# Performance work log

Measured on AMD Instinct MI355X. Metric: run time of the kernel, lower is better.

The kernel has to match this reference:

```python
import jax, jax.numpy as jnp
import numpy as np

N = 50000   # total nodes
E = 600000  # total edges
D = 128     # feature dim (node_dim == all gcn_dims)
G = 128     # graphs in batch
LN_EPS = 1e-5


def setup_inputs() -> dict:
    key = jax.random.key(0)
    ks = jax.random.split(key, 16)
    inp = {
        "x": jax.random.normal(ks[0], (N, D), dtype=jnp.float32),
        "edge_index": jax.random.randint(ks[1], (2, E), 0, N),
        "batch": jnp.sort(jax.random.randint(ks[2], (N,), 0, G)),
    }
    for l in range(3):
        inp[f"W{l}"] = jax.random.normal(ks[3 + 4 * l], (D, D), dtype=jnp.float32) / np.float32(np.sqrt(D))
        inp[f"b{l}"] = jnp.zeros((D,), jnp.float32)
        inp[f"g{l}"] = jnp.ones((D,), jnp.float32)   # LayerNorm weight
        inp[f"be{l}"] = jnp.zeros((D,), jnp.float32)  # LayerNorm bias
    return inp


def _gcn_norm(edge_index):
    # PyG GCNConv default: add self-loops, symmetric deg^-1/2 normalization.
    loop = jnp.arange(N, dtype=edge_index.dtype)
    src = jnp.concatenate([edge_index[0], loop])
    dst = jnp.concatenate([edge_index[1], loop])
    deg = jax.ops.segment_sum(jnp.ones(src.shape[0], jnp.float32), dst, num_segments=N)
    dinv = jnp.where(deg > 0, jax.lax.rsqrt(deg), 0.0)
    norm = dinv[src] * dinv[dst]  # [E+N]
    return src, dst, norm


def _block(x, src, dst, norm, W, b, g, be):
    # GCNConv: gather-transform-scatter
    h = x @ W                                   # [N, D]
    msg = h[src] * norm[:, None]                # [E+N, D] gather + scale
    out = jax.ops.segment_sum(msg, dst, num_segments=N) + b
    # LayerNorm
    mu = jnp.mean(out, axis=-1, keepdims=True)
    var = jnp.mean((out - mu) ** 2, axis=-1, keepdims=True)
    out = (out - mu) * jax.lax.rsqrt(var + LN_EPS) * g + be
    # residual (Identity since in==out channels) + SiLU
    return jax.nn.silu(out + x)


def reference(x, edge_index, batch, W0, b0, g0, be0, W1, b1, g1, be1, W2, b2, g2, be2):
    src, dst, norm = _gcn_norm(edge_index)
    params = [(W0, b0, g0, be0), (W1, b1, g1, be1), (W2, b2, g2, be2)]
    for (W, b, g, be) in params:
        x = _block(x, src, dst, norm, W, b, g, be)
    # global mean pool over batch ids
    counts = jax.ops.segment_sum(jnp.ones((N,), jnp.float32), batch, num_segments=G)
    sums = jax.ops.segment_sum(x, batch, num_segments=G)
    return sums / jnp.maximum(counts, 1.0)[:, None]
```

## Files before the change

kernel.cpp:

```cpp
#include <hip/hip_runtime.h>
#include <math.h>

#define DD 128

typedef __attribute__((ext_vector_type(8))) short short8;
typedef __attribute__((ext_vector_type(4))) float f32x4;

__device__ __forceinline__ unsigned short f2b(float f) {
    unsigned int x = __float_as_uint(f);
    return (unsigned short)((x + 0x7FFFu + ((x >> 16) & 1u)) >> 16);
}
__device__ __forceinline__ float b2f(unsigned short u) {
    return __uint_as_float(((unsigned int)u) << 16);
}

__global__ __launch_bounds__(256) void k_count(const int* __restrict__ dst, int* __restrict__ cnt, int E) {
    int e = blockIdx.x * 256 + threadIdx.x;
    if (e < E) atomicAdd(&cnt[dst[e]], 1);
}

__global__ __launch_bounds__(256) void k_scan1(const int* __restrict__ cnt, int* __restrict__ part, int N) {
    __shared__ int lds[256];
    int t = threadIdx.x;
    int i = blockIdx.x * 256 + t;
    lds[t] = (i < N) ? cnt[i] : 0;
    __syncthreads();
#pragma unroll
    for (int off = 128; off > 0; off >>= 1) {
        if (t < off) lds[t] += lds[t + off];
        __syncthreads();
    }
    if (t == 0) part[blockIdx.x] = lds[0];
}

__global__ __launch_bounds__(1024) void k_scan2(int* __restrict__ part, int* __restrict__ rowptr,
                                                int nblk, int N) {
    __shared__ int lds[1024];
    int t = threadIdx.x;
    int v = (t < nblk) ? part[t] : 0;
    lds[t] = v;
    __syncthreads();
    for (int off = 1; off < 1024; off <<= 1) {
        int u = (t >= off) ? lds[t - off] : 0;
        __syncthreads();
        lds[t] += u;
        __syncthreads();
    }
    if (t < nblk) part[t] = lds[t] - v;
    if (t == 1023) rowptr[N] = lds[1023];
}

__global__ __launch_bounds__(256) void k_scan3(const int* __restrict__ cnt, const int* __restrict__ part,
                                               int* __restrict__ rowptr, int N) {
    __shared__ int lds[256];
    int t = threadIdx.x;
    int i = blockIdx.x * 256 + t;
    int v = (i < N) ? cnt[i] : 0;
    lds[t] = v;
    __syncthreads();
    for (int off = 1; off < 256; off <<= 1) {
        int u = (t >= off) ? lds[t - off] : 0;
        __syncthreads();
        lds[t] += u;
        __syncthreads();
    }
    if (i < N) rowptr[i] = part[blockIdx.x] + lds[t] - v;
}

__global__ __launch_bounds__(256) void k_dinv(const int* __restrict__ cnt, float* __restrict__ dinv, int N) {
    int i = blockIdx.x * 256 + threadIdx.x;
    if (i < N) dinv[i] = rsqrtf((float)cnt[i] + 1.0f);
}

__global__ __launch_bounds__(256) void k_fill(const int* __restrict__ src, const int* __restrict__ dst,
                                              const float* __restrict__ dinv, const int* __restrict__ rowptr,
                                              int* __restrict__ cursor, int2* __restrict__ adj, int E) {
    int e = blockIdx.x * 256 + threadIdx.x;
    if (e >= E) return;
    int s = src[e], d = dst[e];
    int pos = atomicAdd(&cursor[d], 1);
    float w = dinv[s] * dinv[d];
    adj[rowptr[d] + pos] = make_int2(s, __float_as_int(w));
}

__global__ __launch_bounds__(256) void k_prepW(const float* __restrict__ W, unsigned short* __restrict__ WT) {
    int idx = blockIdx.x * 256 + threadIdx.x;
    int k = idx >> 7, c = idx & 127;
    WT[c * DD + k] = f2b(W[idx]);
}

__global__ __launch_bounds__(256) void k_gemm_mfma(const float* __restrict__ X,
                                                   const unsigned short* __restrict__ WT,
                                                   unsigned short* __restrict__ H, int N) {
    __shared__ __align__(16) unsigned short sB[DD * DD];
    __shared__ __align__(16) unsigned short sA[64 * DD];
    int tid = threadIdx.x;
    long row0 = (long)blockIdx.x * 64;

#pragma unroll
    for (int i = 0; i < 8; ++i) {
        int q = tid + 256 * i;
        int c = q >> 4, j = q & 15;
        short8 v = *(const short8*)(WT + q * 8);
        int byte = c * 256 + ((j * 16) ^ ((c & 7) << 4));
        *(short8*)((char*)sB + byte) = v;
    }
#pragma unroll
    for (int i = 0; i < 4; ++i) {
        int q = tid + 256 * i;
        int r = q >> 4, j = q & 15;
        float4 a0 = make_float4(0.f, 0.f, 0.f, 0.f), a1 = a0;
        if (row0 + r < N) {
            const float4* p = (const float4*)(X + (row0 + r) * DD + j * 8);
            a0 = p[0];
            a1 = p[1];
        }
        short8 v;
        v[0] = (short)f2b(a0.x); v[1] = (short)f2b(a0.y);
        v[2] = (short)f2b(a0.z); v[3] = (short)f2b(a0.w);
        v[4] = (short)f2b(a1.x); v[5] = (short)f2b(a1.y);
        v[6] = (short)f2b(a1.z); v[7] = (short)f2b(a1.w);
        int byte = r * 256 + ((j * 16) ^ ((r & 7) << 4));
        *(short8*)((char*)sA + byte) = v;
    }
    __syncthreads();

    int w = tid >> 6, l = tid & 63;
    int lr = l & 15, kg = l >> 4;
    f32x4 acc[8] = {};

#pragma unroll
    for (int step = 0; step < 4; ++step) {
        int ar = w * 16 + lr;
        int abyte = ar * 256 + ((step * 64 + kg * 16) ^ ((ar & 7) << 4));
        short8 af = *(const short8*)((const char*)sA + abyte);
#pragma unroll
        for (int ct = 0; ct < 8; ++ct) {
            int c = ct * 16 + lr;
            int bbyte = c * 256 + ((step * 64 + kg * 16) ^ ((c & 7) << 4));
            short8 bf = *(const short8*)((const char*)sB + bbyte);
            acc[ct] = __builtin_amdgcn_mfma_f32_16x16x32_bf16(af, bf, acc[ct], 0, 0, 0);
        }
    }

#pragma unroll
    for (int ct = 0; ct < 8; ++ct) {
#pragma unroll
        for (int reg = 0; reg < 4; ++reg) {
            long r = row0 + w * 16 + kg * 4 + reg;
            if (r < N) H[r * DD + ct * 16 + lr] = f2b(acc[ct][reg]);
        }
    }
}

__global__ __launch_bounds__(256) void k_agg(const unsigned short* __restrict__ h, const float* __restrict__ xin,
                                             const int* __restrict__ rowptr, const int2* __restrict__ adj,
                                             const float* __restrict__ dinv, const float* __restrict__ b,
                                             const float* __restrict__ g, const float* __restrict__ be,
                                             float* __restrict__ xout, int N) {
    int row = blockIdx.x * 4 + (threadIdx.x >> 6);
    if (row >= N) return;
    int lane = threadIdx.x & 63;
    const unsigned int* hu = (const unsigned int*)h;

    float dv = dinv[row];
    float dv2 = dv * dv;
    unsigned int us = hu[(size_t)row * 64 + lane];
    float2 bv = ((const float2*)b)[lane];
    float2 acc = make_float2(fmaf(b2f((unsigned short)(us & 0xFFFF)), dv2, bv.x),
                             fmaf(b2f((unsigned short)(us >> 16)), dv2, bv.y));

    int beg = rowptr[row], end = rowptr[row + 1];
    for (int j0 = beg; j0 < end; j0 += 64) {
        int myj = j0 + lane;
        int2 a = make_int2(0, 0);
        if (myj < end) a = adj[myj];
        int cnt = min(64, end - j0);
        int cntR = (cnt + 7) & ~7;
        for (int k0 = 0; k0 < cntR; k0 += 8) {
            unsigned int un[8];
            float wt[8];
#pragma unroll
            for (int u = 0; u < 8; ++u) {
                int s = __shfl(a.x, k0 + u, 64);
                wt[u] = __int_as_float(__shfl(a.y, k0 + u, 64));
                un[u] = hu[(size_t)s * 64 + lane];
            }
#pragma unroll
            for (int u = 0; u < 8; ++u) {
                acc.x = fmaf(wt[u], b2f((unsigned short)(un[u] & 0xFFFF)), acc.x);
                acc.y = fmaf(wt[u], b2f((unsigned short)(un[u] >> 16)), acc.y);
            }
        }
    }

    float ssum = acc.x + acc.y;
#pragma unroll
    for (int o = 32; o > 0; o >>= 1) ssum += __shfl_xor(ssum, o, 64);
    float mu = ssum * (1.0f / 128.0f);
    float dx0 = acc.x - mu, dx1 = acc.y - mu;
    float vs = dx0 * dx0 + dx1 * dx1;
#pragma unroll
    for (int o = 32; o > 0; o >>= 1) vs += __shfl_xor(vs, o, 64);
    float rstd = rsqrtf(vs * (1.0f / 128.0f) + 1e-5f);

    float2 gv = ((const float2*)g)[lane];
    float2 bev = ((const float2*)be)[lane];
    float2 xv = ((const float2*)(xin + (size_t)row * DD))[lane];
    float a0 = fmaf(dx0 * rstd, gv.x, bev.x) + xv.x;
    float a1 = fmaf(dx1 * rstd, gv.y, bev.y) + xv.y;
    a0 = a0 / (1.0f + expf(-a0));
    a1 = a1 / (1.0f + expf(-a1));
    ((float2*)(xout + (size_t)row * DD))[lane] = make_float2(a0, a1);
}

__global__ __launch_bounds__(256) void k_pool2(const float* __restrict__ x, const int* __restrict__ batch,
                                               float* __restrict__ out, int N) {
    int gi = blockIdx.x;
    int lo = 0, hi = N;
    while (lo < hi) { int m = (lo + hi) >> 1; if (batch[m] < gi) lo = m + 1; else hi = m; }
    int beg = lo;
    lo = beg; hi = N;
    while (lo < hi) { int m = (lo + hi) >> 1; if (batch[m] < gi + 1) lo = m + 1; else hi = m; }
    int end = lo;

    int tid = threadIdx.x;
    int wave = tid >> 6, lane = tid & 63;
    float2 acc = make_float2(0.f, 0.f);
    for (int r = beg + wave; r < end; r += 4) {
        float2 v = ((const float2*)(x + (size_t)r * DD))[lane];
        acc.x += v.x;
        acc.y += v.y;
    }
    __shared__ float part[4][DD];
    ((float2*)part[wave])[lane] = acc;
    __syncthreads();
    if (wave == 0) {
        float sx = 0.f, sy = 0.f;
#pragma unroll
        for (int w = 0; w < 4; ++w) {
            float2 v = ((const float2*)part[w])[lane];
            sx += v.x;
            sy += v.y;
        }
        float inv = 1.0f / fmaxf((float)(end - beg), 1.0f);
        ((float2*)(out + (size_t)gi * DD))[lane] = make_float2(sx * inv, sy * inv);
    }
}

extern "C" void kernel_launch(void* const* d_in, const int* in_sizes, int n_in,
                              void* d_out, int out_size, void* d_ws, size_t ws_size,
                              hipStream_t stream) {
    const float* x = (const float*)d_in[0];
    const int* edge = (const int*)d_in[1];
    const int* batch = (const int*)d_in[2];
    const float* W[3] = {(const float*)d_in[3], (const float*)d_in[7], (const float*)d_in[11]};
    const float* b[3] = {(const float*)d_in[4], (const float*)d_in[8], (const float*)d_in[12]};
    const float* g[3] = {(const float*)d_in[5], (const float*)d_in[9], (const float*)d_in[13]};
    const float* be[3] = {(const float*)d_in[6], (const float*)d_in[10], (const float*)d_in[14]};

    int N = in_sizes[0] / DD;
    int E = in_sizes[1] / 2;
    int G = out_size / DD;
    const int* srcI = edge;
    const int* dstI = edge + E;

    int nblk = (N + 255) / 256;

    char* ws = (char*)d_ws;
    size_t ND = (size_t)N * DD;
    float* bufX = (float*)ws;                         ws += ND * 4;
    unsigned short* bufH = (unsigned short*)ws;       ws += ND * 2;
    unsigned short* wt[3];
    for (int l = 0; l < 3; ++l) { wt[l] = (unsigned short*)ws; ws += (size_t)DD * DD * 2; }
    float* dinv = (float*)ws;                         ws += (size_t)N * 4;
    int* cnt = (int*)ws;                              ws += (size_t)N * 4;
    int* cursor = (int*)ws;                           ws += (size_t)N * 4;
    int* rowptr = (int*)ws;                           ws += (size_t)(N + 1) * 4;
    int* part = (int*)ws;                             ws += (size_t)nblk * 4;
    ws = (char*)(((uintptr_t)ws + 15) & ~(uintptr_t)15);
    int2* adj = (int2*)ws;

    hipMemsetAsync(cnt, 0, (size_t)N * 2 * 4, stream);

    k_count<<<(E + 255) / 256, 256, 0, stream>>>(dstI, cnt, E);
    k_scan1<<<nblk, 256, 0, stream>>>(cnt, part, N);
    k_scan2<<<1, 1024, 0, stream>>>(part, rowptr, nblk, N);
    k_scan3<<<nblk, 256, 0, stream>>>(cnt, part, rowptr, N);
    k_dinv<<<(N + 255) / 256, 256, 0, stream>>>(cnt, dinv, N);
    k_fill<<<(E + 255) / 256, 256, 0, stream>>>(srcI, dstI, dinv, rowptr, cursor, adj, E);
    for (int l = 0; l < 3; ++l)
        k_prepW<<<64, 256, 0, stream>>>(W[l], wt[l]);

    const float* xin = x;
    for (int l = 0; l < 3; ++l) {
        k_gemm_mfma<<<(N + 63) / 64, 256, 0, stream>>>(xin, wt[l], bufH, N);
        k_agg<<<(N + 3) / 4, 256, 0, stream>>>(bufH, xin, rowptr, adj, dinv, b[l], g[l], be[l], bufX, N);
        xin = bufX;
    }

    k_pool2<<<G, 256, 0, stream>>>(bufX, batch, (float*)d_out, N);
}
```

Baseline: 248.3 us.

## Store inter-layer activations in bf16 and merge small setup kernels

The activation buffer written by the aggregation kernel changes from fp32 to packed bf16. The next GEMM, the residual read and the final pooling now read bf16 directly, which halves activation traffic and removes the fp32-to-bf16 conversion in the GEMM load. The dinv computation is folded into the last scan kernel, and the three weight-prep launches become one, cutting launch count. The cost is lower precision in the residual path and pooled output, and layers 1 and 2 now update the activation buffer in place.

Result: faster. 240.8 us (-3.0%).

```diff
diff --git a/kernel.cpp b/kernel.cpp
--- a/kernel.cpp
+++ b/kernel.cpp
@@ -51,7 +51,7 @@
 }
 
 __global__ __launch_bounds__(256) void k_scan3(const int* __restrict__ cnt, const int* __restrict__ part,
-                                               int* __restrict__ rowptr, int N) {
+                                               int* __restrict__ rowptr, float* __restrict__ dinv, int N) {
     __shared__ int lds[256];
     int t = threadIdx.x;
     int i = blockIdx.x * 256 + t;
@@ -64,12 +64,10 @@
         lds[t] += u;
         __syncthreads();
     }
-    if (i < N) rowptr[i] = part[blockIdx.x] + lds[t] - v;
-}
-
-__global__ __launch_bounds__(256) void k_dinv(const int* __restrict__ cnt, float* __restrict__ dinv, int N) {
-    int i = blockIdx.x * 256 + threadIdx.x;
-    if (i < N) dinv[i] = rsqrtf((float)cnt[i] + 1.0f);
+    if (i < N) {
+        rowptr[i] = part[blockIdx.x] + lds[t] - v;
+        dinv[i] = rsqrtf((float)v + 1.0f);
+    }
 }
 
 __global__ __launch_bounds__(256) void k_fill(const int* __restrict__ src, const int* __restrict__ dst,
@@ -83,13 +81,19 @@
     adj[rowptr[d] + pos] = make_int2(s, __float_as_int(w));
 }
 
-__global__ __launch_bounds__(256) void k_prepW(const float* __restrict__ W, unsigned short* __restrict__ WT) {
-    int idx = blockIdx.x * 256 + threadIdx.x;
+__global__ __launch_bounds__(256) void k_prepW3(const float* __restrict__ W0, const float* __restrict__ W1,
+                                                const float* __restrict__ W2, unsigned short* __restrict__ T0,
+                                                unsigned short* __restrict__ T1, unsigned short* __restrict__ T2) {
+    int l = blockIdx.x >> 6;
+    const float* W = (l == 0) ? W0 : (l == 1) ? W1 : W2;
+    unsigned short* WT = (l == 0) ? T0 : (l == 1) ? T1 : T2;
+    int idx = (blockIdx.x & 63) * 256 + threadIdx.x;
     int k = idx >> 7, c = idx & 127;
     WT[c * DD + k] = f2b(W[idx]);
 }
 
-__global__ __launch_bounds__(256) void k_gemm_mfma(const float* __restrict__ X,
+template <int IN_BF16>
+__global__ __launch_bounds__(256) void k_gemm_mfma(const void* __restrict__ Xv,
                                                    const unsigned short* __restrict__ WT,
                                                    unsigned short* __restrict__ H, int N) {
     __shared__ __align__(16) unsigned short sB[DD * DD];
@@ -109,17 +113,23 @@
     for (int i = 0; i < 4; ++i) {
         int q = tid + 256 * i;
         int r = q >> 4, j = q & 15;
-        float4 a0 = make_float4(0.f, 0.f, 0.f, 0.f), a1 = a0;
-        if (row0 + r < N) {
-            const float4* p = (const float4*)(X + (row0 + r) * DD + j * 8);
-            a0 = p[0];
-            a1 = p[1];
-        }
         short8 v;
-        v[0] = (short)f2b(a0.x); v[1] = (short)f2b(a0.y);
-        v[2] = (short)f2b(a0.z); v[3] = (short)f2b(a0.w);
-        v[4] = (short)f2b(a1.x); v[5] = (short)f2b(a1.y);
-        v[6] = (short)f2b(a1.z); v[7] = (short)f2b(a1.w);
+        if (IN_BF16) {
+#pragma unroll
+            for (int z = 0; z < 8; ++z) v[z] = 0;
+            if (row0 + r < N) v = *(const short8*)((const unsigned short*)Xv + (row0 + r) * DD + j * 8);
+        } else {
+            float4 a0 = make_float4(0.f, 0.f, 0.f, 0.f), a1 = a0;
+            if (row0 + r < N) {
+                const float4* p = (const float4*)((const float*)Xv + (row0 + r) * DD + j * 8);
+                a0 = p[0];
+                a1 = p[1];
+            }
+            v[0] = (short)f2b(a0.x); v[1] = (short)f2b(a0.y);
+            v[2] = (short)f2b(a0.z); v[3] = (short)f2b(a0.w);
+            v[4] = (short)f2b(a1.x); v[5] = (short)f2b(a1.y);
+            v[6] = (short)f2b(a1.z); v[7] = (short)f2b(a1.w);
+        }
         int byte = r * 256 + ((j * 16) ^ ((r & 7) << 4));
         *(short8*)((char*)sA + byte) = v;
     }
@@ -153,11 +163,12 @@
     }
 }
 
-__global__ __launch_bounds__(256) void k_agg(const unsigned short* __restrict__ h, const float* __restrict__ xin,
+template <int IN_BF16>
+__global__ __launch_bounds__(256) void k_agg(const unsigned short* __restrict__ h, const void* __restrict__ xin,
                                              const int* __restrict__ rowptr, const int2* __restrict__ adj,
                                              const float* __restrict__ dinv, const float* __restrict__ b,
                                              const float* __restrict__ g, const float* __restrict__ be,
-                                             float* __restrict__ xout, int N) {
+                                             unsigned int* __restrict__ xout, int N) {
     int row = blockIdx.x * 4 + (threadIdx.x >> 6);
     if (row >= N) return;
     int lane = threadIdx.x & 63;
@@ -206,15 +217,21 @@
 
     float2 gv = ((const float2*)g)[lane];
     float2 bev = ((const float2*)be)[lane];
-    float2 xv = ((const float2*)(xin + (size_t)row * DD))[lane];
+    float2 xv;
+    if (IN_BF16) {
+        unsigned int xu = ((const unsigned int*)xin)[(size_t)row * 64 + lane];
+        xv = make_float2(b2f((unsigned short)(xu & 0xFFFF)), b2f((unsigned short)(xu >> 16)));
+    } else {
+        xv = ((const float2*)xin)[(size_t)row * 64 + lane];
+    }
     float a0 = fmaf(dx0 * rstd, gv.x, bev.x) + xv.x;
     float a1 = fmaf(dx1 * rstd, gv.y, bev.y) + xv.y;
     a0 = a0 / (1.0f + expf(-a0));
     a1 = a1 / (1.0f + expf(-a1));
-    ((float2*)(xout + (size_t)row * DD))[lane] = make_float2(a0, a1);
-}
-
-__global__ __launch_bounds__(256) void k_pool2(const float* __restrict__ x, const int* __restrict__ batch,
+    xout[(size_t)row * 64 + lane] = ((unsigned int)f2b(a1) << 16) | (unsigned int)f2b(a0);
+}
+
+__global__ __launch_bounds__(256) void k_pool2(const unsigned int* __restrict__ x, const int* __restrict__ batch,
                                                float* __restrict__ out, int N) {
     int gi = blockIdx.x;
     int lo = 0, hi = N;
@@ -228,9 +245,9 @@
     int wave = tid >> 6, lane = tid & 63;
     float2 acc = make_float2(0.f, 0.f);
     for (int r = beg + wave; r < end; r += 4) {
-        float2 v = ((const float2*)(x + (size_t)r * DD))[lane];
-        acc.x += v.x;
-        acc.y += v.y;
+        unsigned int u = x[(size_t)r * 64 + lane];
+        acc.x += b2f((unsigned short)(u & 0xFFFF));
+        acc.y += b2f((unsigned short)(u >> 16));
     }
     __shared__ float part[4][DD];
     ((float2*)part[wave])[lane] = acc;
@@ -269,7 +286,7 @@
 
     char* ws = (char*)d_ws;
     size_t ND = (size_t)N * DD;
-    float* bufX = (float*)ws;                         ws += ND * 4;
+    unsigned int* bufX = (unsigned int*)ws;           ws += ND * 2;
     unsigned short* bufH = (unsigned short*)ws;       ws += ND * 2;
     unsigned short* wt[3];
     for (int l = 0; l < 3; ++l) { wt[l] = (unsigned short*)ws; ws += (size_t)DD * DD * 2; }
@@ -286,17 +303,16 @@
     k_count<<<(E + 255) / 256, 256, 0, stream>>>(dstI, cnt, E);
     k_scan1<<<nblk, 256, 0, stream>>>(cnt, part, N);
     k_scan2<<<1, 1024, 0, stream>>>(part, rowptr, nblk, N);
-    k_scan3<<<nblk, 256, 0, stream>>>(cnt, part, rowptr, N);
-    k_dinv<<<(N + 255) / 256, 256, 0, stream>>>(cnt, dinv, N);
+    k_scan3<<<nblk, 256, 0, stream>>>(cnt, part, rowptr, dinv, N);
     k_fill<<<(E + 255) / 256, 256, 0, stream>>>(srcI, dstI, dinv, rowptr, cursor, adj, E);
-    for (int l = 0; l < 3; ++l)
-        k_prepW<<<64, 256, 0, stream>>>(W[l], wt[l]);
-
-    const float* xin = x;
-    for (int l = 0; l < 3; ++l) {
-        k_gemm_mfma<<<(N + 63) / 64, 256, 0, stream>>>(xin, wt[l], bufH, N);
-        k_agg<<<(N + 3) / 4, 256, 0, stream>>>(bufH, xin, rowptr, adj, dinv, b[l], g[l], be[l], bufX, N);
-        xin = bufX;
+    k_prepW3<<<192, 256, 0, stream>>>(W[0], W[1], W[2], wt[0], wt[1], wt[2]);
+
+    int gblk = (N + 63) / 64, ablk = (N + 3) / 4;
+    k_gemm_mfma<0><<<gblk, 256, 0, stream>>>(x, wt[0], bufH, N);
+    k_agg<0><<<ablk, 256, 0, stream>>>(bufH, x, rowptr, adj, dinv, b[0], g[0], be[0], bufX, N);
+    for (int l = 1; l < 3; ++l) {
+        k_gemm_mfma<1><<<gblk, 256, 0, stream>>>(bufX, wt[l], bufH, N);
+        k_agg<1><<<ablk, 256, 0, stream>>>(bufH, bufX, rowptr, adj, dinv, b[l], g[l], be[l], bufX, N);
     }
 
     k_pool2<<<G, 256, 0, stream>>>(bufX, batch, (float*)d_out, N);
```
